# Optimization experiments

Hardware: AMD Instinct MI355X
Metric: run time of the kernel (lower is better)

Reference implementation:

```python
import jax, jax.numpy as jnp
import numpy as np

B, SEQ, H = 128, 400, 1024
STYLE, NMEL, T = 320, 80, 2000


def _lstm_cell(x, h, c, W_ih, W_hh, b_ih, b_hh):
    # torch LSTMCell gate order: i, f, g, o
    gates = x @ W_ih.T + b_ih + h @ W_hh.T + b_hh
    i, f, g, o = jnp.split(gates, 4, axis=-1)
    c_new = jax.nn.sigmoid(f) * c + jax.nn.sigmoid(i) * jnp.tanh(g)
    h_new = jax.nn.sigmoid(o) * jnp.tanh(c_new)
    return h_new, c_new


def setup_inputs() -> dict:
    key = jax.random.key(0)
    ks = jax.random.split(key, 14)
    in1 = H + STYLE + NMEL  # lstm1 input size
    k1 = 1.0 / np.sqrt(H)
    u = lambda k, shape: jax.random.uniform(k, shape, jnp.float32, -k1, k1)
    return {
        "enc_out": jax.random.normal(ks[0], (B, SEQ, H), jnp.float32),
        "style_emb": jax.random.normal(ks[1], (B, STYLE), jnp.float32),
        "mel_tgt": jax.random.normal(ks[2], (B, NMEL, T), jnp.float32),
        "W_ih1": u(ks[3], (4 * H, in1)),
        "W_hh1": u(ks[4], (4 * H, H)),
        "b_ih1": u(ks[5], (4 * H,)),
        "b_hh1": u(ks[6], (4 * H,)),
        "W_ih2": u(ks[7], (4 * H, H)),
        "W_hh2": u(ks[8], (4 * H, H)),
        "b_ih2": u(ks[9], (4 * H,)),
        "b_hh2": u(ks[10], (4 * H,)),
        "fc_w": u(ks[11], (NMEL, H)),
        "fc_b": u(ks[12], (NMEL,)),
    }


def reference(enc_out, style_emb, mel_tgt, W_ih1, W_hh1, b_ih1, b_hh1,
              W_ih2, W_hh2, b_ih2, b_hh2, fc_w, fc_b):
    b, n_mels, t_len = mel_tgt.shape
    seq_len = enc_out.shape[1]
    hid = W_hh1.shape[1]
    # txt_vector per step: enc_out[:, min(t, seq_len-1), :]
    idx = jnp.minimum(jnp.arange(t_len), seq_len - 1)
    txt = jnp.transpose(enc_out[:, idx, :], (1, 0, 2))  # [T, B, H]
    # teacher forcing: prev at step t is mel_tgt[:, :, t-1], zeros at t=0
    prev = jnp.concatenate(
        [jnp.zeros((b, n_mels, 1), mel_tgt.dtype), mel_tgt[:, :, :-1]], axis=2)
    prev = jnp.transpose(prev, (2, 0, 1))  # [T, B, NMEL]

    def step(carry, xs):
        h1, c1, h2, c2 = carry
        txt_t, prev_t = xs
        inp = jnp.concatenate([txt_t, style_emb, prev_t], axis=1)
        h1, c1 = _lstm_cell(inp, h1, c1, W_ih1, W_hh1, b_ih1, b_hh1)
        h2, c2 = _lstm_cell(h1, h2, c2, W_ih2, W_hh2, b_ih2, b_hh2)
        frame = h2 @ fc_w.T + fc_b  # [B, NMEL]
        return (h1, c1, h2, c2), frame

    z = jnp.zeros((b, hid), enc_out.dtype)
    _, frames = jax.lax.scan(step, (z, z, z, z), (txt, prev))  # [T, B, NMEL]
    return jnp.transpose(frames, (1, 2, 0))  # [B, NMEL, T]
```

## Files before the change

### kernel.cpp

```cpp
#include <hip/hip_runtime.h>
#include <hip/hip_bf16.h>
#include <stdint.h>


#define NSUP 2003

typedef __attribute__((ext_vector_type(8))) short bf16x8;
typedef __attribute__((ext_vector_type(4))) float f32x4;

#define OFF_WTXT   0ull
#define OFF_WHH1   8388608ull
#define OFF_WPREV  16777216ull
#define OFF_WIH2   17825792ull
#define OFF_WHH2   26214400ull
#define OFF_FCW    34603008ull
#define OFF_BIAS2  34799616ull
#define OFF_PS_H1R 34816000ull
#define OFF_ENC    36913152ull
#define OFF_STYLET 141606912ull
#define OFF_PREV   141770752ull
#define OFF_H2     208093184ull
#define OFF_EPG1   208617472ull
#define OFF_EPG2   208621568ull
#define WS_NEED    208717824ull

__device__ __forceinline__ unsigned short f2bf(float f) {
  __hip_bfloat16 b = __float2bfloat16(f);
  return *reinterpret_cast<unsigned short*>(&b);
}
__device__ __forceinline__ float sigm(float x) { return 1.f / (1.f + __expf(-x)); }
__device__ __forceinline__ float tanh_(float x) {
  x = fminf(15.f, fmaxf(-15.f, x));
  float e = __expf(2.f * x);
  return (e - 1.f) / (e + 1.f);
}
__device__ __forceinline__ int origRow(int rp) {
  return ((rp >> 4) & 3) * 1024 + (rp >> 6) * 16 + (rp & 15);
}

#define VMW(n) asm volatile("s_waitcnt vmcnt(" #n ")" ::: "memory")

__device__ __forceinline__ void ldx4(bf16x8& d, const void* p) {
  asm volatile("global_load_dwordx4 %0, %1, off" : "=v"(d) : "v"(p));
}
__device__ __forceinline__ void ldx4a(bf16x8& d, const void* p) {
  asm volatile("global_load_dwordx4 %0, %1, off sc1" : "=v"(d) : "v"(p));
}

__device__ __forceinline__ size_t fragOff(int c, int n) {
  return (size_t)(c >> 6) * 131072 + (size_t)(n >> 8) * 32768 +
         (size_t)((n >> 5) & 7) * 4096 + (size_t)((c >> 4) & 3) * 1024 +
         (size_t)((((n >> 3) & 3) * 16) + (c & 15)) * 16 + (size_t)(n & 7) * 2;
}

__global__ void k_pack_w1(const float* __restrict__ wih1, const float* __restrict__ whh1,
                          unsigned char* __restrict__ ws) {
  int idx = blockIdx.x * 256 + threadIdx.x;
  int rp = idx >> 10, k = idx & 1023;
  int orig = origRow(rp);
  ((unsigned short*)(ws + OFF_WTXT))[idx] = f2bf(wih1[(size_t)orig * 1424 + k]);
  ((unsigned short*)(ws + OFF_WHH1))[idx] = f2bf(whh1[(size_t)orig * 1024 + k]);
}
__global__ void k_pack_w2(const float* __restrict__ wih2, const float* __restrict__ whh2,
                          unsigned char* __restrict__ ws) {
  int idx = blockIdx.x * 256 + threadIdx.x;
  int rp = idx >> 10, k = idx & 1023;
  int orig = origRow(rp);
  ((unsigned short*)(ws + OFF_WIH2))[idx] = f2bf(wih2[(size_t)orig * 1024 + k]);
  ((unsigned short*)(ws + OFF_WHH2))[idx] = f2bf(whh2[(size_t)orig * 1024 + k]);
}
__global__ void k_bias2(const float* __restrict__ bih2, const float* __restrict__ bhh2,
                        unsigned char* __restrict__ ws) {
  int rp = blockIdx.x * 256 + threadIdx.x;
  if (rp >= 4096) return;
  int orig = origRow(rp);
  ((float*)(ws + OFF_BIAS2))[rp] = bih2[orig] + bhh2[orig];
}
__global__ void k_pack_wprev(const float* __restrict__ wih1, unsigned char* __restrict__ ws) {
  int idx = blockIdx.x * 256 + threadIdx.x;
  int rp = idx >> 7, k = idx & 127;
  int orig = origRow(rp);
  ((unsigned short*)(ws + OFF_WPREV))[idx] =
      (k < 80) ? f2bf(wih1[(size_t)orig * 1424 + 1344 + k]) : (unsigned short)0;
}
__global__ void k_pack_fc(const float* __restrict__ fcw, unsigned char* __restrict__ ws) {
  int idx = blockIdx.x * 256 + threadIdx.x;
  int r = idx >> 10, k = idx & 1023;
  ((unsigned short*)(ws + OFF_FCW))[idx] =
      (r < 80) ? f2bf(fcw[(size_t)r * 1024 + k]) : (unsigned short)0;
}
__global__ void k_pack_enc(const float* __restrict__ enc, unsigned char* __restrict__ ws) {
  size_t i = (size_t)blockIdx.x * 256 + threadIdx.x;
  float4 v = ((const float4*)enc)[i];
  union { unsigned short u[4]; unsigned long long ll; } z;
  z.u[0] = f2bf(v.x); z.u[1] = f2bf(v.y); z.u[2] = f2bf(v.z); z.u[3] = f2bf(v.w);
  int b  = (int)(i / (400 * 256));
  int tp = (int)((i >> 8) % 400);
  int u4 = (int)(i & 255);
  *(unsigned long long*)(ws + OFF_ENC + (size_t)tp * 262144 + fragOff(b, u4 * 4)) = z.ll;
}
__global__ void k_styleT(const float* __restrict__ style, float* __restrict__ sT) {
  int idx = blockIdx.x * 256 + threadIdx.x;
  int j = idx >> 7, n = idx & 127;
  sT[idx] = style[n * 320 + j];
}
__global__ void k_pstyle(const float* __restrict__ wih1, const float* __restrict__ bih1,
                         const float* __restrict__ bhh1, const float* __restrict__ sT,
                         unsigned char* __restrict__ ws) {
  int n = threadIdx.x & 127, rsub = threadIdx.x >> 7;
  int rp = blockIdx.x * 2 + rsub;
  int orig = origRow(rp);
  const float* wr = wih1 + (size_t)orig * 1424 + 1024;
  float a0 = 0.f, a1 = 0.f, a2 = 0.f, a3 = 0.f;
  for (int j = 0; j < 320; j += 4) {
    a0 += wr[j + 0] * sT[(j + 0) * 128 + n];
    a1 += wr[j + 1] * sT[(j + 1) * 128 + n];
    a2 += wr[j + 2] * sT[(j + 2) * 128 + n];
    a3 += wr[j + 3] * sT[(j + 3) * 128 + n];
  }
  ((float*)(ws + OFF_PS_H1R))[rp * 128 + n] = (a0 + a1) + (a2 + a3) + bih1[orig] + bhh1[orig];
}
__global__ void k_pack_prev(const float* __restrict__ mel, unsigned char* __restrict__ ws) {
  __shared__ unsigned short pl[64][80];
  int b = blockIdx.y, tt0 = blockIdx.x * 64;
  int tid = threadIdx.x;
  int ttl = tid & 63, mi = tid >> 6;
  for (int m = mi; m < 80; m += 4) {
    int tau = tt0 + ttl;
    if (tau <= 1998) pl[ttl][m] = f2bf(mel[((size_t)b * 80 + m) * 2000 + tau]);
  }
  __syncthreads();
  for (int idx = tid; idx < 64 * 80; idx += 256) {
    int t2 = idx / 80, m = idx % 80;
    int tau = tt0 + t2;
    if (tau <= 1998) {
      size_t off = (size_t)(tau + 1) * 32768 + (size_t)(b >> 6) * 16384 +
                   (size_t)(m >> 5) * 4096 + (size_t)((b >> 4) & 3) * 1024 +
                   (size_t)((((m >> 3) & 3) * 16) + (b & 15)) * 16 + (size_t)(m & 7) * 2;
      *(unsigned short*)(ws + OFF_PREV + off) = pl[t2][m];
    }
  }
}

__global__ __launch_bounds__(256, 1) void k_persist(unsigned char* __restrict__ ws,
                                                    float* __restrict__ out,
                                                    const float* __restrict__ fc_b) {
  __shared__ float red[4][64][68];
  __shared__ float fcred[4][16][68];

  const int tid = threadIdx.x, bid = blockIdx.x;
  const int w = tid >> 6, l = tid & 63;
  const int r15 = l & 15, khi = l >> 4;
  const bool isG1 = bid < 128;
  const int lb = bid & 127, rb = lb >> 1, cg = lb & 1;
  const bool fcB = (!isG1) && (lb < 12);
  const int u6 = lb >> 1;
  const int ecol = tid & 63, quad = tid >> 6;

  bf16x8 avr[4][16];
  bf16x8 avp[4];
#pragma unroll
  for (int i = 0; i < 4; ++i) {
    const size_t row = (size_t)(rb * 64 + 16 * i + r15);
    const unsigned char* pa =
        ws + (isG1 ? OFF_WTXT : OFF_WIH2) + row * 2048 + w * 512 + khi * 16;
    const unsigned char* ph =
        ws + (isG1 ? OFF_WHH1 : OFF_WHH2) + row * 2048 + w * 512 + khi * 16;
#pragma unroll
    for (int t = 0; t < 8; ++t) avr[i][t] = *(const bf16x8*)(pa + t * 64);
#pragma unroll
    for (int t = 0; t < 8; ++t) avr[i][8 + t] = *(const bf16x8*)(ph + t * 64);
    if (isG1)
      avp[i] = *(const bf16x8*)(ws + OFF_WPREV + row * 256 + w * 64 + khi * 16);
  }
  bf16x8 fcav[8];
  if (fcB) {
    const unsigned char* pf = ws + OFF_FCW + (size_t)(u6 * 16 + r15) * 2048 + w * 512 + khi * 16;
#pragma unroll
    for (int t = 0; t < 8; ++t) fcav[t] = *(const bf16x8*)(pf + t * 64);
  }
  float pstb[4][4];
  if (isG1) {
    const float* PS = (const float*)(ws + OFF_PS_H1R);
#pragma unroll
    for (int g = 0; g < 4; ++g)
#pragma unroll
      for (int u = 0; u < 4; ++u)
        pstb[g][u] = PS[(size_t)(rb * 64 + 16 * g + quad * 4 + u) * 128 + cg * 64 + ecol];
  }

  const size_t hfragOff = (size_t)cg * 131072 + (size_t)(rb >> 4) * 32768 +
                          (size_t)((rb >> 1) & 7) * 4096 + (size_t)(ecol >> 4) * 1024 +
                          (size_t)((((rb & 1) * 2 + (quad >> 1)) * 16) + (ecol & 15)) * 16 +
                          (size_t)(quad & 1) * 8;
  const size_t cfrag = (size_t)cg * 131072 + (size_t)w * 32768 + (size_t)l * 16;

  float fcbr[4];
#pragma unroll
  for (int q = 0; q < 4; ++q) {
    int m = u6 * 16 + quad * 4 + q;
    fcbr[q] = (fcB && m < 80) ? fc_b[m] : 0.f;
  }
  float cst[4] = {0.f, 0.f, 0.f, 0.f};
  const f32x4 zero4 = {0.f, 0.f, 0.f, 0.f};

  unsigned* myslot = (unsigned*)(ws + (isG1 ? OFF_EPG1 : OFF_EPG2) +
                                 (size_t)(cg * 64 + rb) * 4);
  auto epPub = [&](unsigned v) __attribute__((always_inline)) {
    __hip_atomic_store(myslot, v, __ATOMIC_RELEASE, __HIP_MEMORY_SCOPE_AGENT);
  };
  const unsigned* q1 = (const unsigned*)(ws + OFF_EPG1 + (size_t)(cg * 64 + l) * 4);
  const unsigned* q2 = (const unsigned*)(ws + OFF_EPG2 + (size_t)(cg * 64 + l) * 4);
  auto waitSlots = [&](unsigned t1, unsigned t2) __attribute__((always_inline)) {
    if (w == 0) {
      for (long it = 0; it < 4000000; ++it) {
        unsigned v1 = __hip_atomic_load(q1, __ATOMIC_RELAXED, __HIP_MEMORY_SCOPE_AGENT);
        unsigned v2 = __hip_atomic_load(q2, __ATOMIC_RELAXED, __HIP_MEMORY_SCOPE_AGENT);
        if (__all((v1 >= t1) && (v2 >= t2))) break;
        __builtin_amdgcn_s_sleep(2);
      }
    }
    __syncthreads();
  };

  __syncthreads();
  if (tid == 0) epPub(1u);

  {
    if (w == 0) {
      const unsigned* a0 = (const unsigned*)(ws + OFF_EPG1 + (size_t)l * 4);
      const unsigned* a1 = (const unsigned*)(ws + OFF_EPG1 + (size_t)(64 + l) * 4);
      const unsigned* b0 = (const unsigned*)(ws + OFF_EPG2 + (size_t)l * 4);
      const unsigned* b1 = (const unsigned*)(ws + OFF_EPG2 + (size_t)(64 + l) * 4);
      for (long it = 0; it < 8000000; ++it) {
        unsigned v0 = __hip_atomic_load(a0, __ATOMIC_RELAXED, __HIP_MEMORY_SCOPE_AGENT);
        unsigned v1 = __hip_atomic_load(a1, __ATOMIC_RELAXED, __HIP_MEMORY_SCOPE_AGENT);
        unsigned v2 = __hip_atomic_load(b0, __ATOMIC_RELAXED, __HIP_MEMORY_SCOPE_AGENT);
        unsigned v3 = __hip_atomic_load(b1, __ATOMIC_RELAXED, __HIP_MEMORY_SCOPE_AGENT);
        if (__all((v0 >= 1u) && (v1 >= 1u) && (v2 >= 1u) && (v3 >= 1u))) break;
        __builtin_amdgcn_s_sleep(2);
      }
    }
    __syncthreads();
  }

  bf16x8 bvr[4][4];

#pragma unroll 1
  for (int s = 0; s < NSUP; ++s) {
    const bool g1a = isG1 && (s <= 1999);
    const bool g2a = (!isG1) && (s >= 2) && (s <= 2001);
    const bool fca = fcB && (s >= 3) && (s <= 2002);
    const bool g2run = g2a || fca;

    if (g1a) {
      f32x4 acc[4][4];
#pragma unroll
      for (int i = 0; i < 4; ++i)
#pragma unroll
        for (int j = 0; j < 4; ++j) acc[i][j] = zero4;

      const int tp = (s < 399) ? s : 399;
      const unsigned char* encw = ws + OFF_ENC + (size_t)tp * 262144 + cfrag;
      const unsigned char* prvw = ws + OFF_PREV + (size_t)s * 32768 +
                                  (size_t)cg * 16384 + (size_t)w * 4096 + (size_t)l * 16;
      const unsigned char *ep[4], *pp[4];
#pragma unroll
      for (int j = 0; j < 4; ++j) { ep[j] = encw + j * 1024; pp[j] = prvw + j * 1024; }
      auto ISSs = [&](int t) __attribute__((always_inline)) {
        if (t < 8) {
#pragma unroll
          for (int j = 0; j < 4; ++j) { ldx4(bvr[t & 3][j], ep[j]); ep[j] += 4096; }
        } else {
#pragma unroll
          for (int j = 0; j < 4; ++j) ldx4(bvr[t & 3][j], pp[j]);
        }
      };
      ISSs(0); ISSs(1); ISSs(2); ISSs(3);
#pragma unroll
      for (int t = 0; t < 9; ++t) {
        if (t <= 5) VMW(12);
        else if (t == 6) VMW(8);
        else if (t == 7) VMW(4);
        else VMW(0);
        __builtin_amdgcn_sched_barrier(0);
#pragma unroll
        for (int i = 0; i < 4; ++i)
#pragma unroll
          for (int j = 0; j < 4; ++j)
            acc[i][j] = __builtin_amdgcn_mfma_f32_16x16x32_bf16(
                (t < 8) ? avr[i][t] : avp[i], bvr[t & 3][j], acc[i][j], 0, 0, 0);
        if (t + 4 <= 8) ISSs(t + 4);
      }

      {
        unsigned t2 = (s >= 5) ? (unsigned)(s - 4) : 1u;
        waitSlots((unsigned)(s + 1), t2);
      }

      if (s > 0) {
        const unsigned char* h1w_ = ws + OFF_PS_H1R + (size_t)((s - 1) & 7) * 262144 + cfrag;
        const unsigned char* hp[4];
#pragma unroll
        for (int j = 0; j < 4; ++j) hp[j] = h1w_ + j * 1024;
        auto ISSh = [&](int t) __attribute__((always_inline)) {
#pragma unroll
          for (int j = 0; j < 4; ++j) { ldx4a(bvr[t & 3][j], hp[j]); hp[j] += 4096; }
        };
        ISSh(0); ISSh(1); ISSh(2); ISSh(3);
#pragma unroll
        for (int t = 0; t < 8; ++t) {
          if (t <= 4) VMW(12);
          else if (t == 5) VMW(8);
          else if (t == 6) VMW(4);
          else VMW(0);
          __builtin_amdgcn_sched_barrier(0);
#pragma unroll
          for (int i = 0; i < 4; ++i)
#pragma unroll
            for (int j = 0; j < 4; ++j)
              acc[i][j] = __builtin_amdgcn_mfma_f32_16x16x32_bf16(avr[i][8 + t], bvr[t & 3][j],
                                                                  acc[i][j], 0, 0, 0);
          if (t + 4 <= 7) ISSh(t + 4);
        }
      }

#pragma unroll
      for (int i = 0; i < 4; ++i)
#pragma unroll
        for (int j = 0; j < 4; ++j)
#pragma unroll
          for (int q = 0; q < 4; ++q)
            red[w][16 * i + khi * 4 + q][16 * j + r15] = acc[i][j][q];
      __syncthreads();
      {
        unsigned hm[4];
#pragma unroll
        for (int u = 0; u < 4; ++u) {
          float gt[4];
#pragma unroll
          for (int g = 0; g < 4; ++g) {
            int row = 16 * g + quad * 4 + u;
            gt[g] = red[0][row][ecol] + red[1][row][ecol] + red[2][row][ecol] +
                    red[3][row][ecol] + pstb[g][u];
          }
          float ci = sigm(gt[0]), cf = sigm(gt[1]), cgt = tanh_(gt[2]), co = sigm(gt[3]);
          cst[u] = cf * cst[u] + ci * cgt;
          hm[u] = f2bf(co * tanh_(cst[u]));
        }
        unsigned long long hv = (unsigned long long)(hm[0] | (hm[1] << 16)) |
                                ((unsigned long long)(hm[2] | (hm[3] << 16)) << 32);
        const void* ha = ws + OFF_PS_H1R + (size_t)(s & 7) * 262144 + hfragOff;
        asm volatile("global_store_dwordx2 %0, %1, off sc1" ::"v"(ha), "v"(hv) : "memory");
      }
    } else if (g2run) {
      waitSlots((unsigned)s, (unsigned)(s + 1));

      f32x4 acc[4][4];
      f32x4 facc[4];
#pragma unroll
      for (int i = 0; i < 4; ++i) {
        facc[i] = zero4;
#pragma unroll
        for (int j = 0; j < 4; ++j) acc[i][j] = zero4;
      }
      const unsigned char *p1[4], *p2[4];
      {
        const unsigned char* h1rd = ws + OFF_PS_H1R + (size_t)((s - 2) & 7) * 262144 + cfrag;
        const unsigned char* h2rd = ws + OFF_H2 + (size_t)((s + 1) & 1) * 262144 + cfrag;
#pragma unroll
        for (int j = 0; j < 4; ++j) { p1[j] = h1rd + j * 1024; p2[j] = h2rd + j * 1024; }
      }
      auto ISS2 = [&](int t) __attribute__((always_inline)) {
        if (t < 8) {
#pragma unroll
          for (int j = 0; j < 4; ++j) { ldx4a(bvr[t & 3][j], p1[j]); p1[j] += 4096; }
        } else {
#pragma unroll
          for (int j = 0; j < 4; ++j) { ldx4a(bvr[t & 3][j], p2[j]); p2[j] += 4096; }
        }
      };
      ISS2(0); ISS2(1); ISS2(2); ISS2(3);
#pragma unroll
      for (int t = 0; t < 16; ++t) {
        if (t <= 12) VMW(12);
        else if (t == 13) VMW(8);
        else if (t == 14) VMW(4);
        else VMW(0);
        __builtin_amdgcn_sched_barrier(0);
        if (g2a) {
#pragma unroll
          for (int i = 0; i < 4; ++i)
#pragma unroll
            for (int j = 0; j < 4; ++j)
              acc[i][j] = __builtin_amdgcn_mfma_f32_16x16x32_bf16(avr[i][t], bvr[t & 3][j],
                                                                  acc[i][j], 0, 0, 0);
        }
        if (fca && t >= 8) {
#pragma unroll
          for (int j = 0; j < 4; ++j)
            facc[j] = __builtin_amdgcn_mfma_f32_16x16x32_bf16(fcav[t - 8], bvr[t & 3][j],
                                                              facc[j], 0, 0, 0);
        }
        if (t + 4 <= 15) ISS2(t + 4);
      }

      if (g2a) {
#pragma unroll
        for (int i = 0; i < 4; ++i)
#pragma unroll
          for (int j = 0; j < 4; ++j)
#pragma unroll
            for (int q = 0; q < 4; ++q)
              red[w][16 * i + khi * 4 + q][16 * j + r15] = acc[i][j][q];
      }
      if (fca) {
#pragma unroll
        for (int j = 0; j < 4; ++j)
#pragma unroll
          for (int q = 0; q < 4; ++q)
            fcred[w][khi * 4 + q][16 * j + r15] = facc[j][q];
      }
      __syncthreads();
      if (g2a) {
        const float* B2 = (const float*)(ws + OFF_BIAS2);
        float pb[4][4];
#pragma unroll
        for (int g = 0; g < 4; ++g)
#pragma unroll
          for (int u = 0; u < 4; ++u)
            pb[g][u] = B2[rb * 64 + 16 * g + quad * 4 + u];
        unsigned hm[4];
#pragma unroll
        for (int u = 0; u < 4; ++u) {
          float gt[4];
#pragma unroll
          for (int g = 0; g < 4; ++g) {
            int row = 16 * g + quad * 4 + u;
            gt[g] = red[0][row][ecol] + red[1][row][ecol] + red[2][row][ecol] +
                    red[3][row][ecol] + pb[g][u];
          }
          float ci = sigm(gt[0]), cf = sigm(gt[1]), cgt = tanh_(gt[2]), co = sigm(gt[3]);
          cst[u] = cf * cst[u] + ci * cgt;
          hm[u] = f2bf(co * tanh_(cst[u]));
        }
        unsigned long long hv = (unsigned long long)(hm[0] | (hm[1] << 16)) |
                                ((unsigned long long)(hm[2] | (hm[3] << 16)) << 32);
        const void* ha = ws + OFF_H2 + (size_t)(s & 1) * 262144 + hfragOff;
        asm volatile("global_store_dwordx2 %0, %1, off sc1" ::"v"(ha), "v"(hv) : "memory");
      }
      if (fca) {
        const int t0 = s - 3;
#pragma unroll
        for (int q = 0; q < 4; ++q) {
          int m = u6 * 16 + quad * 4 + q;
          float v = fcred[0][quad * 4 + q][ecol] + fcred[1][quad * 4 + q][ecol] +
                    fcred[2][quad * 4 + q][ecol] + fcred[3][quad * 4 + q][ecol] + fcbr[q];
          if (m < 80) out[((size_t)(cg * 64 + ecol) * 80 + m) * 2000 + t0] = v;
        }
      }
    }

    VMW(0);
    __syncthreads();
    if (tid == 0) epPub((unsigned)(s + 2));
  }
}

extern "C" void kernel_launch(void* const* d_in, const int* in_sizes, int n_in,
                              void* d_out, int out_size, void* d_ws, size_t ws_size,
                              hipStream_t stream) {
  (void)in_sizes; (void)n_in; (void)out_size;
  const float* enc  = (const float*)d_in[0];
  const float* styl = (const float*)d_in[1];
  const float* mel  = (const float*)d_in[2];
  const float* Wih1 = (const float*)d_in[3];
  const float* Whh1 = (const float*)d_in[4];
  const float* bih1 = (const float*)d_in[5];
  const float* bhh1 = (const float*)d_in[6];
  const float* Wih2 = (const float*)d_in[7];
  const float* Whh2 = (const float*)d_in[8];
  const float* bih2 = (const float*)d_in[9];
  const float* bhh2 = (const float*)d_in[10];
  const float* fcw  = (const float*)d_in[11];
  const float* fcb  = (const float*)d_in[12];
  unsigned char* ws = (unsigned char*)d_ws;
  float* out = (float*)d_out;
  if (ws_size < WS_NEED) return;

  hipMemsetAsync(ws + OFF_PREV, 0, (size_t)(WS_NEED - OFF_PREV), stream);
  k_pack_w1<<<16384, 256, 0, stream>>>(Wih1, Whh1, ws);
  k_pack_w2<<<16384, 256, 0, stream>>>(Wih2, Whh2, ws);
  k_bias2<<<16, 256, 0, stream>>>(bih2, bhh2, ws);
  k_pack_wprev<<<2048, 256, 0, stream>>>(Wih1, ws);
  k_pack_fc<<<384, 256, 0, stream>>>(fcw, ws);
  k_styleT<<<160, 256, 0, stream>>>(styl, (float*)(ws + OFF_STYLET));
  k_pstyle<<<2048, 256, 0, stream>>>(Wih1, bih1, bhh1, (float*)(ws + OFF_STYLET), ws);
  k_pack_enc<<<51200, 256, 0, stream>>>(enc, ws);
  k_pack_prev<<<dim3(32, 128), 256, 0, stream>>>(mel, ws);
  k_persist<<<256, 256, 0, stream>>>(ws, out, fcb);
}
```

Measured before the change: 26.69 ms.

## Replace per-block slot waits with per-wave waits and stream h-state via global_load_lds

```diff
diff --git a/kernel.cpp b/kernel.cpp
--- a/kernel.cpp
+++ b/kernel.cpp
@@ -7,6 +7,8 @@
 
 typedef __attribute__((ext_vector_type(8))) short bf16x8;
 typedef __attribute__((ext_vector_type(4))) float f32x4;
+typedef const __attribute__((address_space(1))) unsigned int* GPTR;
+typedef __attribute__((address_space(3))) unsigned int* LPTR;
 
 #define OFF_WTXT   0ull
 #define OFF_WHH1   8388608ull
@@ -43,9 +45,6 @@
 __device__ __forceinline__ void ldx4(bf16x8& d, const void* p) {
   asm volatile("global_load_dwordx4 %0, %1, off" : "=v"(d) : "v"(p));
 }
-__device__ __forceinline__ void ldx4a(bf16x8& d, const void* p) {
-  asm volatile("global_load_dwordx4 %0, %1, off sc1" : "=v"(d) : "v"(p));
-}
 
 __device__ __forceinline__ size_t fragOff(int c, int n) {
   return (size_t)(c >> 6) * 131072 + (size_t)(n >> 8) * 32768 +
@@ -145,8 +144,9 @@
 __global__ __launch_bounds__(256, 1) void k_persist(unsigned char* __restrict__ ws,
                                                     float* __restrict__ out,
                                                     const float* __restrict__ fc_b) {
-  __shared__ float red[4][64][68];
-  __shared__ float fcred[4][16][68];
+  __shared__ __align__(1024) unsigned char smem[131072];
+  float (*red)[64][68] = (float(*)[64][68])smem;
+  float (*fcred)[16][68] = (float(*)[16][68])(smem + 69632);
 
   const int tid = threadIdx.x, bid = blockIdx.x;
   const int w = tid >> 6, l = tid & 63;
@@ -193,7 +193,8 @@
                           (size_t)((rb >> 1) & 7) * 4096 + (size_t)(ecol >> 4) * 1024 +
                           (size_t)((((rb & 1) * 2 + (quad >> 1)) * 16) + (ecol & 15)) * 16 +
                           (size_t)(quad & 1) * 8;
-  const size_t cfrag = (size_t)cg * 131072 + (size_t)w * 32768 + (size_t)l * 16;
+  const size_t cfragW = (size_t)cg * 131072 + (size_t)w * 32768;
+  unsigned char* landW = smem + w * 32768;
 
   float fcbr[4];
 #pragma unroll
@@ -209,18 +210,18 @@
   auto epPub = [&](unsigned v) __attribute__((always_inline)) {
     __hip_atomic_store(myslot, v, __ATOMIC_RELEASE, __HIP_MEMORY_SCOPE_AGENT);
   };
-  const unsigned* q1 = (const unsigned*)(ws + OFF_EPG1 + (size_t)(cg * 64 + l) * 4);
-  const unsigned* q2 = (const unsigned*)(ws + OFF_EPG2 + (size_t)(cg * 64 + l) * 4);
-  auto waitSlots = [&](unsigned t1, unsigned t2) __attribute__((always_inline)) {
-    if (w == 0) {
-      for (long it = 0; it < 4000000; ++it) {
-        unsigned v1 = __hip_atomic_load(q1, __ATOMIC_RELAXED, __HIP_MEMORY_SCOPE_AGENT);
-        unsigned v2 = __hip_atomic_load(q2, __ATOMIC_RELAXED, __HIP_MEMORY_SCOPE_AGENT);
-        if (__all((v1 >= t1) && (v2 >= t2))) break;
-        __builtin_amdgcn_s_sleep(2);
-      }
+  const unsigned* pw1 = (const unsigned*)(ws + OFF_EPG1 +
+                         (size_t)(cg * 64 + w * 16 + (l & 15)) * 4);
+  const unsigned* pw2 = (const unsigned*)(ws + OFF_EPG2 +
+                         (size_t)(cg * 64 + w * 16 + (l & 15)) * 4);
+  auto waitWave = [&](unsigned t1, unsigned t2) __attribute__((always_inline)) {
+    for (long it = 0; it < 8000000; ++it) {
+      unsigned v1 = __hip_atomic_load(pw1, __ATOMIC_RELAXED, __HIP_MEMORY_SCOPE_AGENT);
+      unsigned v2 = __hip_atomic_load(pw2, __ATOMIC_RELAXED, __HIP_MEMORY_SCOPE_AGENT);
+      bool ok = (l < 16) ? (v1 >= t1) : (l < 32) ? (v2 >= t2) : true;
+      if (__all(ok)) break;
+      __builtin_amdgcn_s_sleep(1);
     }
-    __syncthreads();
   };
 
   __syncthreads();
@@ -261,7 +262,7 @@
         for (int j = 0; j < 4; ++j) acc[i][j] = zero4;
 
       const int tp = (s < 399) ? s : 399;
-      const unsigned char* encw = ws + OFF_ENC + (size_t)tp * 262144 + cfrag;
+      const unsigned char* encw = ws + OFF_ENC + (size_t)tp * 262144 + cfragW + (size_t)l * 16;
       const unsigned char* prvw = ws + OFF_PREV + (size_t)s * 32768 +
                                   (size_t)cg * 16384 + (size_t)w * 4096 + (size_t)l * 16;
       const unsigned char *ep[4], *pp[4];
@@ -293,38 +294,42 @@
         if (t + 4 <= 8) ISSs(t + 4);
       }
 
-      {
-        unsigned t2 = (s >= 5) ? (unsigned)(s - 4) : 1u;
-        waitSlots((unsigned)(s + 1), t2);
-      }
+      waitWave((unsigned)(s + 1), (s >= 5) ? (unsigned)(s - 4) : 1u);
 
       if (s > 0) {
-        const unsigned char* h1w_ = ws + OFF_PS_H1R + (size_t)((s - 1) & 7) * 262144 + cfrag;
-        const unsigned char* hp[4];
-#pragma unroll
-        for (int j = 0; j < 4; ++j) hp[j] = h1w_ + j * 1024;
-        auto ISSh = [&](int t) __attribute__((always_inline)) {
-#pragma unroll
-          for (int j = 0; j < 4; ++j) { ldx4a(bvr[t & 3][j], hp[j]); hp[j] += 4096; }
-        };
-        ISSh(0); ISSh(1); ISSh(2); ISSh(3);
+        const unsigned char* h1b = ws + OFF_PS_H1R + (size_t)((s - 1) & 7) * 262144 +
+                                   cfragW + (size_t)l * 16;
+#pragma unroll
+        for (int g = 0; g < 8; ++g)
+#pragma unroll
+          for (int j = 0; j < 4; ++j)
+            __builtin_amdgcn_global_load_lds((GPTR)(h1b + g * 4096 + j * 1024),
+                                             (LPTR)(landW + g * 4096 + j * 1024), 16, 0, 17);
 #pragma unroll
         for (int t = 0; t < 8; ++t) {
-          if (t <= 4) VMW(12);
+          if (t == 0) VMW(28);
+          else if (t == 1) VMW(24);
+          else if (t == 2) VMW(20);
+          else if (t == 3) VMW(16);
+          else if (t == 4) VMW(12);
           else if (t == 5) VMW(8);
           else if (t == 6) VMW(4);
           else VMW(0);
           __builtin_amdgcn_sched_barrier(0);
+          bf16x8 bv[4];
+#pragma unroll
+          for (int j = 0; j < 4; ++j)
+            bv[j] = *(const bf16x8*)(landW + t * 4096 + j * 1024 + l * 16);
 #pragma unroll
           for (int i = 0; i < 4; ++i)
 #pragma unroll
             for (int j = 0; j < 4; ++j)
-              acc[i][j] = __builtin_amdgcn_mfma_f32_16x16x32_bf16(avr[i][8 + t], bvr[t & 3][j],
+              acc[i][j] = __builtin_amdgcn_mfma_f32_16x16x32_bf16(avr[i][8 + t], bv[j],
                                                                   acc[i][j], 0, 0, 0);
-          if (t + 4 <= 7) ISSh(t + 4);
-        }
-      }
-
+        }
+      }
+
+      __syncthreads();
 #pragma unroll
       for (int i = 0; i < 4; ++i)
 #pragma unroll
@@ -354,7 +359,7 @@
         asm volatile("global_store_dwordx2 %0, %1, off sc1" ::"v"(ha), "v"(hv) : "memory");
       }
     } else if (g2run) {
-      waitSlots((unsigned)s, (unsigned)(s + 1));
+      waitWave((unsigned)s, (unsigned)(s + 1));
 
       f32x4 acc[4][4];
       f32x4 facc[4];
@@ -364,47 +369,53 @@
 #pragma unroll
         for (int j = 0; j < 4; ++j) acc[i][j] = zero4;
       }
-      const unsigned char *p1[4], *p2[4];
-      {
-        const unsigned char* h1rd = ws + OFF_PS_H1R + (size_t)((s - 2) & 7) * 262144 + cfrag;
-        const unsigned char* h2rd = ws + OFF_H2 + (size_t)((s + 1) & 1) * 262144 + cfrag;
-#pragma unroll
-        for (int j = 0; j < 4; ++j) { p1[j] = h1rd + j * 1024; p2[j] = h2rd + j * 1024; }
-      }
-      auto ISS2 = [&](int t) __attribute__((always_inline)) {
-        if (t < 8) {
-#pragma unroll
-          for (int j = 0; j < 4; ++j) { ldx4a(bvr[t & 3][j], p1[j]); p1[j] += 4096; }
-        } else {
-#pragma unroll
-          for (int j = 0; j < 4; ++j) { ldx4a(bvr[t & 3][j], p2[j]); p2[j] += 4096; }
-        }
+      const unsigned char* s1 = ws + OFF_PS_H1R + (size_t)((s - 2) & 7) * 262144 +
+                                cfragW + (size_t)l * 16;
+      const unsigned char* s2 = ws + OFF_H2 + (size_t)((s + 1) & 1) * 262144 +
+                                cfragW + (size_t)l * 16;
+      auto ISSL2 = [&](int g) __attribute__((always_inline)) {
+        const unsigned char* src = (g < 8) ? (s1 + g * 4096) : (s2 + (g - 8) * 4096);
+        unsigned char* dst = landW + (g & 7) * 4096;
+#pragma unroll
+        for (int j = 0; j < 4; ++j)
+          __builtin_amdgcn_global_load_lds((GPTR)(src + j * 1024),
+                                           (LPTR)(dst + j * 1024), 16, 0, 17);
       };
-      ISS2(0); ISS2(1); ISS2(2); ISS2(3);
+#pragma unroll
+      for (int g = 0; g < 8; ++g) ISSL2(g);
 #pragma unroll
       for (int t = 0; t < 16; ++t) {
-        if (t <= 12) VMW(12);
+        if (t <= 8) VMW(28);
+        else if (t == 9) VMW(24);
+        else if (t == 10) VMW(20);
+        else if (t == 11) VMW(16);
+        else if (t == 12) VMW(12);
         else if (t == 13) VMW(8);
         else if (t == 14) VMW(4);
         else VMW(0);
         __builtin_amdgcn_sched_barrier(0);
+        bf16x8 bv[4];
+#pragma unroll
+        for (int j = 0; j < 4; ++j)
+          bv[j] = *(const bf16x8*)(landW + (t & 7) * 4096 + j * 1024 + l * 16);
         if (g2a) {
 #pragma unroll
           for (int i = 0; i < 4; ++i)
 #pragma unroll
             for (int j = 0; j < 4; ++j)
-              acc[i][j] = __builtin_amdgcn_mfma_f32_16x16x32_bf16(avr[i][t], bvr[t & 3][j],
+              acc[i][j] = __builtin_amdgcn_mfma_f32_16x16x32_bf16(avr[i][t], bv[j],
                                                                   acc[i][j], 0, 0, 0);
         }
         if (fca && t >= 8) {
 #pragma unroll
           for (int j = 0; j < 4; ++j)
-            facc[j] = __builtin_amdgcn_mfma_f32_16x16x32_bf16(fcav[t - 8], bvr[t & 3][j],
+            facc[j] = __builtin_amdgcn_mfma_f32_16x16x32_bf16(fcav[t - 8], bv[j],
                                                               facc[j], 0, 0, 0);
         }
-        if (t + 4 <= 15) ISS2(t + 4);
-      }
-
+        if (t + 8 <= 15) ISSL2(t + 8);
+      }
+
+      __syncthreads();
       if (g2a) {
 #pragma unroll
         for (int i = 0; i < 4; ++i)
```

After: 31.18 ms. 16.8% more time.

## Add per-XCD gate so one block invalidates L2 before cached h-state loads

Applied to the files above, without the earlier changes.

```diff
diff --git a/kernel.cpp b/kernel.cpp
--- a/kernel.cpp
+++ b/kernel.cpp
@@ -22,6 +22,8 @@
 #define OFF_H2     208093184ull
 #define OFF_EPG1   208617472ull
 #define OFF_EPG2   208621568ull
+#define OFF_XTK    208629760ull
+#define OFF_XEP    208633856ull
 #define WS_NEED    208717824ull
 
 __device__ __forceinline__ unsigned short f2bf(float f) {
@@ -43,8 +45,13 @@
 __device__ __forceinline__ void ldx4(bf16x8& d, const void* p) {
   asm volatile("global_load_dwordx4 %0, %1, off" : "=v"(d) : "v"(p));
 }
-__device__ __forceinline__ void ldx4a(bf16x8& d, const void* p) {
-  asm volatile("global_load_dwordx4 %0, %1, off sc1" : "=v"(d) : "v"(p));
+__device__ __forceinline__ void ldx4s(bf16x8& d, const void* p) {
+  asm volatile("global_load_dwordx4 %0, %1, off sc0" : "=v"(d) : "v"(p));
+}
+__device__ __forceinline__ unsigned getXcd() {
+  unsigned x;
+  asm volatile("s_getreg_b32 %0, hwreg(HW_REG_XCC_ID)" : "=s"(x));
+  return x & 7u;
 }
 
 __device__ __forceinline__ size_t fragOff(int c, int n) {
@@ -156,6 +163,8 @@
   const bool fcB = (!isG1) && (lb < 12);
   const int u6 = lb >> 1;
   const int ecol = tid & 63, quad = tid >> 6;
+  const int ring = isG1 ? 0 : 1;
+  const unsigned xcd = getXcd();
 
   bf16x8 avr[4][16];
   bf16x8 avp[4];
@@ -222,6 +231,32 @@
     }
     __syncthreads();
   };
+  unsigned* xepp = (unsigned*)(ws + OFF_XEP + (size_t)(ring * 8 + xcd) * 64);
+  auto xcdGate = [&](int s) __attribute__((always_inline)) {
+    if (tid == 0) {
+      unsigned* tk = (unsigned*)(ws + OFF_XTK +
+                                 (size_t)((ring * 8 + xcd) * 4 + (s & 3)) * 64);
+      unsigned ticket =
+          __hip_atomic_fetch_add(tk, 1u, __ATOMIC_RELAXED, __HIP_MEMORY_SCOPE_AGENT);
+      if (ticket == 0) {
+        __builtin_amdgcn_fence(__ATOMIC_ACQUIRE, "agent");
+        asm volatile("s_waitcnt vmcnt(0)" ::: "memory");
+        __hip_atomic_store((unsigned*)(ws + OFF_XTK +
+                           (size_t)((ring * 8 + xcd) * 4 + ((s + 2) & 3)) * 64),
+                           0u, __ATOMIC_RELAXED, __HIP_MEMORY_SCOPE_AGENT);
+        __hip_atomic_store(xepp, (unsigned)(s + 1), __ATOMIC_RELEASE,
+                           __HIP_MEMORY_SCOPE_AGENT);
+      } else {
+        for (long it = 0; it < 8000000; ++it) {
+          if (__hip_atomic_load(xepp, __ATOMIC_RELAXED, __HIP_MEMORY_SCOPE_AGENT) >=
+              (unsigned)(s + 1))
+            break;
+          __builtin_amdgcn_s_sleep(1);
+        }
+      }
+    }
+    __syncthreads();
+  };
 
   __syncthreads();
   if (tid == 0) epPub(1u);
@@ -297,6 +332,7 @@
         unsigned t2 = (s >= 5) ? (unsigned)(s - 4) : 1u;
         waitSlots((unsigned)(s + 1), t2);
       }
+      xcdGate(s);
 
       if (s > 0) {
         const unsigned char* h1w_ = ws + OFF_PS_H1R + (size_t)((s - 1) & 7) * 262144 + cfrag;
@@ -305,7 +341,7 @@
         for (int j = 0; j < 4; ++j) hp[j] = h1w_ + j * 1024;
         auto ISSh = [&](int t) __attribute__((always_inline)) {
 #pragma unroll
-          for (int j = 0; j < 4; ++j) { ldx4a(bvr[t & 3][j], hp[j]); hp[j] += 4096; }
+          for (int j = 0; j < 4; ++j) { ldx4s(bvr[t & 3][j], hp[j]); hp[j] += 4096; }
         };
         ISSh(0); ISSh(1); ISSh(2); ISSh(3);
 #pragma unroll
@@ -355,6 +391,7 @@
       }
     } else if (g2run) {
       waitSlots((unsigned)s, (unsigned)(s + 1));
+      xcdGate(s);
 
       f32x4 acc[4][4];
       f32x4 facc[4];
@@ -374,10 +411,10 @@
       auto ISS2 = [&](int t) __attribute__((always_inline)) {
         if (t < 8) {
 #pragma unroll
-          for (int j = 0; j < 4; ++j) { ldx4a(bvr[t & 3][j], p1[j]); p1[j] += 4096; }
+          for (int j = 0; j < 4; ++j) { ldx4s(bvr[t & 3][j], p1[j]); p1[j] += 4096; }
         } else {
 #pragma unroll
-          for (int j = 0; j < 4; ++j) { ldx4a(bvr[t & 3][j], p2[j]); p2[j] += 4096; }
+          for (int j = 0; j < 4; ++j) { ldx4s(bvr[t & 3][j], p2[j]); p2[j] += 4096; }
         }
       };
       ISS2(0); ISS2(1); ISS2(2); ISS2(3);
@@ -456,7 +493,10 @@
           int m = u6 * 16 + quad * 4 + q;
           float v = fcred[0][quad * 4 + q][ecol] + fcred[1][quad * 4 + q][ecol] +
                     fcred[2][quad * 4 + q][ecol] + fcred[3][quad * 4 + q][ecol] + fcbr[q];
-          if (m < 80) out[((size_t)(cg * 64 + ecol) * 80 + m) * 2000 + t0] = v;
+          if (m < 80) {
+            const float* oa = &out[((size_t)(cg * 64 + ecol) * 80 + m) * 2000 + t0];
+            asm volatile("global_store_dword %0, %1, off sc1" ::"v"(oa), "v"(v) : "memory");
+          }
         }
       }
     }
```

Result: slower. 31.59 ms (+18.3%).
